# Kernel tuning notes

Measured on AMD Instinct MI355X. Metric: run time of the kernel, lower is better.

The kernel has to match this reference:

```python
import jax, jax.numpy as jnp
import numpy as np

N = 100000
E = 1600000
F_IN = 128
H1, C1 = 8, 8          # conv1: heads=8, hidden_channels=8 -> concat dim 64
H2, C2 = 1, 40         # conv2: heads=1, out=num_classes=40, concat=False
NEG_SLOPE = 0.2
EPS = 1e-16


def setup_inputs() -> dict:
    key = jax.random.key(0)
    ks = jax.random.split(key, 10)
    x = jax.random.normal(ks[0], (N, F_IN), dtype=jnp.float32)
    edge_index = jax.random.randint(ks[1], (2, E), 0, N, dtype=jnp.int32)
    s1 = 1.0 / np.sqrt(F_IN)
    s2 = 1.0 / np.sqrt(H1 * C1)
    W1 = jax.random.normal(ks[2], (F_IN, H1 * C1), dtype=jnp.float32) * s1
    att_src1 = jax.random.normal(ks[3], (H1, C1), dtype=jnp.float32) * s2
    att_dst1 = jax.random.normal(ks[4], (H1, C1), dtype=jnp.float32) * s2
    b1 = jnp.zeros((H1 * C1,), dtype=jnp.float32)
    W2 = jax.random.normal(ks[5], (H1 * C1, H2 * C2), dtype=jnp.float32) * s2
    att_src2 = jax.random.normal(ks[6], (H2, C2), dtype=jnp.float32) * (1.0 / np.sqrt(C2))
    att_dst2 = jax.random.normal(ks[7], (H2, C2), dtype=jnp.float32) * (1.0 / np.sqrt(C2))
    b2 = jnp.zeros((C2,), dtype=jnpp_zeros_dtype()) if False else jnp.zeros((C2,), dtype=jnp.float32)
    return {"x": x, "W1": W1, "att_src1": att_src1, "att_dst1": att_dst1, "b1": b1,
            "W2": W2, "att_src2": att_src2, "att_dst2": att_dst2, "b2": b2,
            "edge_index": edge_index}


def _gat_conv(x, W, att_src, att_dst, bias, src, dst, num_nodes, concat):
    """PyG GATConv (eval mode, self-loops already added to src/dst)."""
    H, C = att_src.shape
    h = (x @ W).reshape(num_nodes, H, C)                 # [N, H, C]
    a_src = jnp.sum(h * att_src[None], axis=-1)          # [N, H]
    a_dst = jnp.sum(h * att_dst[None], axis=-1)          # [N, H]
    e = a_src[src] + a_dst[dst]                          # [Etot, H]
    e = jax.nn.leaky_relu(e, NEG_SLOPE)
    # segment softmax over incoming edges of each dst node
    e_max = jax.ops.segment_max(e, dst, num_segments=num_nodes)   # [N, H]
    ex = jnp.exp(e - e_max[dst])
    denom = jax.ops.segment_sum(ex, dst, num_segments=num_nodes)  # [N, H]
    alpha = ex / (denom[dst] + EPS)                      # [Etot, H]
    msg = h[src] * alpha[..., None]                      # [Etot, H, C]
    out = jax.ops.segment_sum(msg, dst, num_segments=num_nodes)   # [N, H, C]
    if concat:
        out = out.reshape(num_nodes, H * C)
    else:
        out = out.mean(axis=1)
    return out + bias


def reference(x, W1, att_src1, att_dst1, b1, W2, att_src2, att_dst2, b2, edge_index):
    # add self-loops (PyG GATConv default add_self_loops=True)
    loops = jnp.arange(N, dtype=edge_index.dtype)
    src = jnp.concatenate([edge_index[0], loops])
    dst = jnp.concatenate([edge_index[1], loops])
    # dropout layers are identity in eval mode
    emb = jax.nn.elu(_gat_conv(x, W1, att_src1, att_dst1, b1, src, dst, N, True))
    logits = _gat_conv(emb, W2, att_src2, att_dst2, b2, src, dst, N, False)
    return jax.nn.log_softmax(logits, axis=1), emb


def jnp_zeros_dtype():
    return jnp.float32
```

## Files before the change

kernel.cpp:

```cpp
#include <hip/hip_runtime.h>
#include <hip/hip_fp16.h>
#include <math.h>

#define NN 100000
#define EE 1600000
#define ET (EE + NN)
#define FIN 128
#define D1 64
#define H1 8
#define C1 8
#define C2 40
#define NEG 0.2f
#define EPSV 1e-16f
#define LOG2E 1.4426950408889634f

#define NBKT 196
#define BCAP 10240
#define CHUNK 8192
#define NBB ((ET + CHUNK - 1) / CHUNK)

typedef _Float16 f16x8 __attribute__((ext_vector_type(8)));
typedef float f32x4 __attribute__((ext_vector_type(4)));

__device__ __forceinline__ void edge_sd(int e, const int* __restrict__ ei, int& s, int& d) {
  if (e < EE) { s = ei[e]; d = ei[EE + e]; }
  else        { s = e - EE; d = s; }
}

__global__ __launch_bounds__(256) void scatter_kernel(const int* __restrict__ ei,
                                                      int* __restrict__ gcur,
                                                      int* __restrict__ ecsr) {
  __shared__ int lh[NBKT], lres[NBKT], lcur[NBKT];
  int t = threadIdx.x;
  if (t < NBKT) { lh[t] = 0; lcur[t] = 0; }
  __syncthreads();
  int e0 = blockIdx.x * CHUNK;
  int e1 = min(e0 + CHUNK, ET);
  for (int e = e0 + t; e < e1; e += 256) {
    int d = (e < EE) ? ei[EE + e] : e - EE;
    atomicAdd(&lh[d >> 9], 1);
  }
  __syncthreads();
  if (t < NBKT && lh[t]) lres[t] = atomicAdd(&gcur[t], lh[t]);
  __syncthreads();
  for (int e = e0 + t; e < e1; e += 256) {
    int s, d; edge_sd(e, ei, s, d);
    int b = d >> 9;
    int lp = atomicAdd(&lcur[b], 1);
    ecsr[b * BCAP + lres[b] + lp] = s | ((d & 511) << 17);
  }
}

__global__ __launch_bounds__(256) void bucket2csr_kernel(const int* __restrict__ gcur,
                                                         int2* __restrict__ rowrng,
                                                         int* __restrict__ ecsr) {
  __shared__ int ebuf[BCAP];
  __shared__ int hist[512];
  __shared__ int sd[256];
  int b = blockIdx.x, t = threadIdx.x;
  int base = b * BCAP;
  int cnt = gcur[b];
  hist[t] = 0; hist[t + 256] = 0;
  __syncthreads();
  for (int i = t; i < cnt; i += 256) {
    int p = ecsr[base + i];
    ebuf[i] = p;
    atomicAdd(&hist[p >> 17], 1);
  }
  __syncthreads();
  int h0 = hist[2 * t], h1 = hist[2 * t + 1], s = h0 + h1;
  sd[t] = s;
  __syncthreads();
  for (int off = 1; off < 256; off <<= 1) {
    int x = sd[t];
    int y = (t >= off) ? sd[t - off] : 0;
    __syncthreads();
    sd[t] = x + y;
    __syncthreads();
  }
  int run = sd[t] - s;
  int g = b * 512 + 2 * t;
  if (g < NN)     rowrng[g]     = make_int2(base + run,      base + run + h0);
  if (g + 1 < NN) rowrng[g + 1] = make_int2(base + run + h0, base + run + h0 + h1);
  hist[2 * t] = run;
  hist[2 * t + 1] = run + h0;
  __syncthreads();
  for (int i = t; i < cnt; i += 256) {
    int p = ebuf[i];
    int pos = atomicAdd(&hist[p >> 17], 1);
    ecsr[base + pos] = p & 0x1FFFF;
  }
}

__global__ __launch_bounds__(256) void prep_kernel(
    const float* __restrict__ W1, const float* __restrict__ as1, const float* __restrict__ ad1,
    const float* __restrict__ W2, const float* __restrict__ as2, const float* __restrict__ ad2w,
    __half* __restrict__ Wf1, __half* __restrict__ Wf2) {
  int gid = blockIdx.x * 256 + threadIdx.x;
  int stride = gridDim.x * 256;
  for (int idx = gid; idx < 4 * 5 * 64 * 8; idx += stride) {
    int j = idx & 7, l = (idx >> 3) & 63;
    int g = idx >> 9;
    int ct = g % 5, kk = g / 5;
    int kdim = kk * 32 + (l >> 4) * 8 + j;
    int c = l & 15;
    float v;
    if (ct < 4) v = W1[kdim * 64 + ct * 16 + c];
    else {
      const float* aw = (c < 8) ? as1 : ad1;
      int hh = c & 7;
      float acc = 0.f;
      for (int q = 0; q < 8; ++q) acc += W1[kdim * 64 + hh * 8 + q] * aw[hh * 8 + q];
      v = acc * LOG2E;
    }
    Wf1[idx] = __float2half(v);
  }
  for (int idx = gid; idx < 2 * 3 * 64 * 8; idx += stride) {
    int j = idx & 7, l = (idx >> 3) & 63;
    int g = idx >> 9;
    int ct = g % 3, kk = g / 3;
    int kdim = kk * 32 + (l >> 4) * 8 + j;
    int c = ct * 16 + (l & 15);
    float v = 0.f;
    if (c < C2) v = W2[kdim * C2 + c];
    else if (c == 40 || c == 41) {
      const float* aw = (c == 40) ? as2 : ad2w;
      float acc = 0.f;
      for (int q = 0; q < C2; ++q) acc += W2[kdim * C2 + q] * aw[q];
      v = acc * LOG2E;
    }
    Wf2[idx] = __float2half(v);
  }
}

__global__ __launch_bounds__(256) void gemm1_kernel(
    const float* __restrict__ x, const __half* __restrict__ Wf1,
    __half* __restrict__ h, __half* __restrict__ as_h, float* __restrict__ ad) {
  int t = threadIdx.x;
  int w = t >> 6, lane = t & 63;
  int col = lane & 15, kg = lane >> 4;
  int node0 = blockIdx.x * 64 + w * 16;
  int nodeA = min(node0 + col, NN - 1);
  const float* xr = x + (size_t)nodeA * FIN + kg * 8;
  const f16x8* Wq = (const f16x8*)Wf1;
  f32x4 acc0 = {0.f,0.f,0.f,0.f}, acc1 = acc0, acc2 = acc0, acc3 = acc0, acc4 = acc0;
#pragma unroll
  for (int kk = 0; kk < 4; ++kk) {
    float4 xa = *(const float4*)(xr + kk * 32);
    float4 xb = *(const float4*)(xr + kk * 32 + 4);
    f16x8 a;
    a[0] = (_Float16)xa.x; a[1] = (_Float16)xa.y; a[2] = (_Float16)xa.z; a[3] = (_Float16)xa.w;
    a[4] = (_Float16)xb.x; a[5] = (_Float16)xb.y; a[6] = (_Float16)xb.z; a[7] = (_Float16)xb.w;
    acc0 = __builtin_amdgcn_mfma_f32_16x16x32_f16(a, Wq[(kk * 5 + 0) * 64 + lane], acc0, 0, 0, 0);
    acc1 = __builtin_amdgcn_mfma_f32_16x16x32_f16(a, Wq[(kk * 5 + 1) * 64 + lane], acc1, 0, 0, 0);
    acc2 = __builtin_amdgcn_mfma_f32_16x16x32_f16(a, Wq[(kk * 5 + 2) * 64 + lane], acc2, 0, 0, 0);
    acc3 = __builtin_amdgcn_mfma_f32_16x16x32_f16(a, Wq[(kk * 5 + 3) * 64 + lane], acc3, 0, 0, 0);
    acc4 = __builtin_amdgcn_mfma_f32_16x16x32_f16(a, Wq[(kk * 5 + 4) * 64 + lane], acc4, 0, 0, 0);
  }
#pragma unroll
  for (int reg = 0; reg < 4; ++reg) {
    int nr = node0 + kg * 4 + reg;
    if (nr < NN) {
      h[(size_t)nr * 64 +  0 + col] = __float2half(acc0[reg]);
      h[(size_t)nr * 64 + 16 + col] = __float2half(acc1[reg]);
      h[(size_t)nr * 64 + 32 + col] = __float2half(acc2[reg]);
      h[(size_t)nr * 64 + 48 + col] = __float2half(acc3[reg]);
      float v = acc4[reg];
      if (col < 8) as_h[nr * 8 + col] = __float2half(v);
      else         ad[nr * 8 + col - 8] = v;
    }
  }
}

#define CONS(u, avh, valid) do { \
    float xx = __half2float(avh) + adv; xx = fmaxf(xx, NEG * xx); \
    float e = (valid) ? exp2f(xx) : 0.f; den += e; \
    float2 f; \
    f = __half22float2(*(const __half2*)&(u).x); a0 = fmaf(f.x, e, a0); a1 = fmaf(f.y, e, a1); \
    f = __half22float2(*(const __half2*)&(u).y); a2 = fmaf(f.x, e, a2); a3 = fmaf(f.y, e, a3); \
    f = __half22float2(*(const __half2*)&(u).z); a4 = fmaf(f.x, e, a4); a5 = fmaf(f.y, e, a5); \
    f = __half22float2(*(const __half2*)&(u).w); a6 = fmaf(f.x, e, a6); a7 = fmaf(f.y, e, a7); \
  } while (0)

__global__ __launch_bounds__(256) void agg1_kernel(
    const int2* __restrict__ rowrng, const int* __restrict__ csr,
    const __half* __restrict__ as_h, const float* __restrict__ ad,
    const __half* __restrict__ h, const float* __restrict__ b1,
    float* __restrict__ emb) {
  int t = threadIdx.x;
  int lane = t & 63;
  int o = lane >> 3, k = lane & 7, ob = lane & 56;
  int node = blockIdx.x * 32 + (t >> 6) * 8 + o;
  int2 rr = rowrng[node];
  int beg = rr.x, deg = rr.y - rr.x, degm1 = deg - 1;
  float adv = ad[node * 8 + k];
  float den = 0.f;
  float a0=0.f,a1=0.f,a2=0.f,a3=0.f,a4=0.f,a5=0.f,a6=0.f,a7=0.f;
  uint4 uA[8]; __half vA[8]; int sjA[8];
  int sA = csr[beg + min(k, degm1)];
#pragma unroll
  for (int r = 0; r < 8; ++r) sjA[r] = __shfl(sA, ob + r, 64);
#pragma unroll
  for (int r = 0; r < 8; ++r) {
    uA[r] = *(const uint4*)(h + ((size_t)(uint)sjA[r] << 6) + (k << 3));
    vA[r] = as_h[(uint)sjA[r] * 8u + k];
  }
  for (int i = 0; i < deg; i += 16) {
    int sB = csr[beg + min(i + 8 + k, degm1)];
    int sjB[8];
#pragma unroll
    for (int r = 0; r < 8; ++r) sjB[r] = __shfl(sB, ob + r, 64);
    uint4 uB[8]; __half vB[8];
#pragma unroll
    for (int r = 0; r < 8; ++r) {
      uB[r] = *(const uint4*)(h + ((size_t)(uint)sjB[r] << 6) + (k << 3));
      vB[r] = as_h[(uint)sjB[r] * 8u + k];
    }
#pragma unroll
    for (int r = 0; r < 8; ++r) CONS(uA[r], vA[r], i + r < deg);
    int sA2 = csr[beg + min(i + 16 + k, degm1)];
#pragma unroll
    for (int r = 0; r < 8; ++r) sjA[r] = __shfl(sA2, ob + r, 64);
#pragma unroll
    for (int r = 0; r < 8; ++r) {
      uA[r] = *(const uint4*)(h + ((size_t)(uint)sjA[r] << 6) + (k << 3));
      vA[r] = as_h[(uint)sjA[r] * 8u + k];
    }
#pragma unroll
    for (int r = 0; r < 8; ++r) CONS(uB[r], vB[r], i + 8 + r < deg);
  }
  float4 bv0 = ((const float4*)b1)[2 * k];
  float4 bv1 = ((const float4*)b1)[2 * k + 1];
  float inv = 1.0f / (den + EPSV);
  float v0 = fmaf(a0, inv, bv0.x), v1 = fmaf(a1, inv, bv0.y);
  float v2 = fmaf(a2, inv, bv0.z), v3 = fmaf(a3, inv, bv0.w);
  float v4 = fmaf(a4, inv, bv1.x), v5 = fmaf(a5, inv, bv1.y);
  float v6 = fmaf(a6, inv, bv1.z), v7 = fmaf(a7, inv, bv1.w);
  v0 = v0 > 0.f ? v0 : expm1f(v0); v1 = v1 > 0.f ? v1 : expm1f(v1);
  v2 = v2 > 0.f ? v2 : expm1f(v2); v3 = v3 > 0.f ? v3 : expm1f(v3);
  v4 = v4 > 0.f ? v4 : expm1f(v4); v5 = v5 > 0.f ? v5 : expm1f(v5);
  v6 = v6 > 0.f ? v6 : expm1f(v6); v7 = v7 > 0.f ? v7 : expm1f(v7);
  float4 s0; s0.x = v0; s0.y = v1; s0.z = v2; s0.w = v3;
  float4 s1; s1.x = v4; s1.y = v5; s1.z = v6; s1.w = v7;
  float* ep = emb + (size_t)node * D1 + (k << 3);
  ((float4*)ep)[0] = s0; ((float4*)ep)[1] = s1;
}

__global__ __launch_bounds__(256) void gemm2_kernel(
    const float* __restrict__ emb, const __half* __restrict__ Wf2,
    __half* __restrict__ h2, float* __restrict__ ad2) {
  int t = threadIdx.x;
  int w = t >> 6, lane = t & 63;
  int col = lane & 15, kg = lane >> 4;
  int node0 = blockIdx.x * 64 + w * 16;
  int nodeA = min(node0 + col, NN - 1);
  const float* er = emb + (size_t)nodeA * D1 + kg * 8;
  const f16x8* Wq = (const f16x8*)Wf2;
  f32x4 acc0 = {0.f,0.f,0.f,0.f}, acc1 = acc0, acc2 = acc0;
#pragma unroll
  for (int kk = 0; kk < 2; ++kk) {
    float4 xa = *(const float4*)(er + kk * 32);
    float4 xb = *(const float4*)(er + kk * 32 + 4);
    f16x8 a;
    a[0] = (_Float16)xa.x; a[1] = (_Float16)xa.y; a[2] = (_Float16)xa.z; a[3] = (_Float16)xa.w;
    a[4] = (_Float16)xb.x; a[5] = (_Float16)xb.y; a[6] = (_Float16)xb.z; a[7] = (_Float16)xb.w;
    acc0 = __builtin_amdgcn_mfma_f32_16x16x32_f16(a, Wq[(kk * 3 + 0) * 64 + lane], acc0, 0, 0, 0);
    acc1 = __builtin_amdgcn_mfma_f32_16x16x32_f16(a, Wq[(kk * 3 + 1) * 64 + lane], acc1, 0, 0, 0);
    acc2 = __builtin_amdgcn_mfma_f32_16x16x32_f16(a, Wq[(kk * 3 + 2) * 64 + lane], acc2, 0, 0, 0);
  }
#pragma unroll
  for (int reg = 0; reg < 4; ++reg) {
    int nr = node0 + kg * 4 + reg;
    if (nr < NN) {
      h2[(size_t)nr * 64 +  0 + col] = __float2half(acc0[reg]);
      h2[(size_t)nr * 64 + 16 + col] = __float2half(acc1[reg]);
      float v = acc2[reg];
      if (col < 8)       h2[(size_t)nr * 64 + 32 + col] = __float2half(v);
      else if (col == 8) h2[(size_t)nr * 64 + 40] = __float2half(v);
      else if (col == 9) ad2[nr] = v;
    }
  }
}

__global__ __launch_bounds__(256) void agg2_kernel(
    const int2* __restrict__ rowrng, const int* __restrict__ csr,
    const float* __restrict__ ad, const __half* __restrict__ h2,
    const float* __restrict__ b2, float* __restrict__ out) {
  int t = threadIdx.x;
  int lane = t & 63;
  int o = lane >> 3, k = lane & 7, ob = lane & 56;
  int kc = min(k, 4);
  int node = blockIdx.x * 32 + (t >> 6) * 8 + o;
  int2 rr = rowrng[node];
  int beg = rr.x, deg = rr.y - rr.x, degm1 = deg - 1;
  float adv = ad[node];
  float den = 0.f;
  float a0=0.f,a1=0.f,a2=0.f,a3=0.f,a4=0.f,a5=0.f,a6=0.f,a7=0.f;
  uint4 uA[8]; __half vA[8]; int sjA[8];
  int sA = csr[beg + min(k, degm1)];
#pragma unroll
  for (int r = 0; r < 8; ++r) sjA[r] = __shfl(sA, ob + r, 64);
#pragma unroll
  for (int r = 0; r < 8; ++r) {
    const __half* rp = h2 + ((size_t)(uint)sjA[r] << 6);
    uA[r] = *(const uint4*)(rp + (kc << 3));
    vA[r] = rp[40];
  }
  for (int i = 0; i < deg; i += 16) {
    int sB = csr[beg + min(i + 8 + k, degm1)];
    int sjB[8];
#pragma unroll
    for (int r = 0; r < 8; ++r) sjB[r] = __shfl(sB, ob + r, 64);
    uint4 uB[8]; __half vB[8];
#pragma unroll
    for (int r = 0; r < 8; ++r) {
      const __half* rp = h2 + ((size_t)(uint)sjB[r] << 6);
      uB[r] = *(const uint4*)(rp + (kc << 3));
      vB[r] = rp[40];
    }
#pragma unroll
    for (int r = 0; r < 8; ++r) CONS(uA[r], vA[r], i + r < deg);
    int sA2 = csr[beg + min(i + 16 + k, degm1)];
#pragma unroll
    for (int r = 0; r < 8; ++r) sjA[r] = __shfl(sA2, ob + r, 64);
#pragma unroll
    for (int r = 0; r < 8; ++r) {
      const __half* rp = h2 + ((size_t)(uint)sjA[r] << 6);
      uA[r] = *(const uint4*)(rp + (kc << 3));
      vA[r] = rp[40];
    }
#pragma unroll
    for (int r = 0; r < 8; ++r) CONS(uB[r], vB[r], i + 8 + r < deg);
  }
  float4 bv0 = ((const float4*)b2)[2 * kc];
  float4 bv1 = ((const float4*)b2)[2 * kc + 1];
  float inv = 1.0f / (den + EPSV);
  float v0 = fmaf(a0, inv, bv0.x), v1 = fmaf(a1, inv, bv0.y);
  float v2 = fmaf(a2, inv, bv0.z), v3 = fmaf(a3, inv, bv0.w);
  float v4 = fmaf(a4, inv, bv1.x), v5 = fmaf(a5, inv, bv1.y);
  float v6 = fmaf(a6, inv, bv1.z), v7 = fmaf(a7, inv, bv1.w);
  bool act = (k < 5);
  float m = act ? fmaxf(fmaxf(fmaxf(v0, v1), fmaxf(v2, v3)),
                        fmaxf(fmaxf(v4, v5), fmaxf(v6, v7))) : -INFINITY;
#pragma unroll
  for (int off = 1; off < 8; off <<= 1) m = fmaxf(m, __shfl_xor(m, off, 64));
  float ex = act ? (__expf(v0 - m) + __expf(v1 - m) + __expf(v2 - m) + __expf(v3 - m) +
                    __expf(v4 - m) + __expf(v5 - m) + __expf(v6 - m) + __expf(v7 - m)) : 0.f;
#pragma unroll
  for (int off = 1; off < 8; off <<= 1) ex += __shfl_xor(ex, off, 64);
  if (act) {
    float lls = m + logf(ex);
    float4 s0; s0.x = v0 - lls; s0.y = v1 - lls; s0.z = v2 - lls; s0.w = v3 - lls;
    float4 s1; s1.x = v4 - lls; s1.y = v5 - lls; s1.z = v6 - lls; s1.w = v7 - lls;
    float* op = out + (size_t)node * C2 + (k << 3);
    ((float4*)op)[0] = s0; ((float4*)op)[1] = s1;
  }
}

extern "C" void kernel_launch(void* const* d_in, const int* in_sizes, int n_in,
                              void* d_out, int out_size, void* d_ws, size_t ws_size,
                              hipStream_t stream) {
  const float* x    = (const float*)d_in[0];
  const float* W1   = (const float*)d_in[1];
  const float* as1w = (const float*)d_in[2];
  const float* ad1w = (const float*)d_in[3];
  const float* b1   = (const float*)d_in[4];
  const float* W2   = (const float*)d_in[5];
  const float* as2w = (const float*)d_in[6];
  const float* ad2w = (const float*)d_in[7];
  const float* b2   = (const float*)d_in[8];
  const int*   ei   = (const int*)d_in[9];

  float* out   = (float*)d_out;
  float* outls = out;
  float* emb   = out + (long)NN * C2;

  char* wsb = (char*)d_ws;
  __half* h1   = (__half*)wsb; wsb += sizeof(__half) * (size_t)NN * D1;
  __half* h2   = (__half*)wsb; wsb += sizeof(__half) * ((size_t)NN * 64 + 64);
  __half* ash1 = (__half*)wsb; wsb += sizeof(__half) * (size_t)NN * H1;
  float* adst1 = (float*)wsb; wsb += sizeof(float) * (size_t)NN * H1;
  float* adst2 = (float*)wsb; wsb += sizeof(float) * (size_t)NN;
  int2* rowrng = (int2*)wsb;  wsb += sizeof(int2) * (size_t)NN;
  int* gcur    = (int*)wsb;   wsb += sizeof(int) * (NBKT + 4);
  __half* Wf1  = (__half*)wsb; wsb += sizeof(__half) * 4 * 5 * 64 * 8;
  __half* Wf2  = (__half*)wsb; wsb += sizeof(__half) * 2 * 3 * 64 * 8;
  int* ecsr    = (int*)wsb;   wsb += sizeof(int) * (size_t)NBKT * BCAP;

  prep_kernel<<<16, 256, 0, stream>>>(W1, as1w, ad1w, W2, as2w, ad2w, Wf1, Wf2);
  hipMemsetAsync(gcur, 0, sizeof(int) * (NBKT + 4), stream);
  scatter_kernel<<<NBB, 256, 0, stream>>>(ei, gcur, ecsr);
  bucket2csr_kernel<<<NBKT, 256, 0, stream>>>(gcur, rowrng, ecsr);

  gemm1_kernel<<<(NN + 63) / 64, 256, 0, stream>>>(x, Wf1, h1, ash1, adst1);
  agg1_kernel<<<NN / 32, 256, 0, stream>>>(rowrng, ecsr, ash1, adst1, h1, b1, emb);

  gemm2_kernel<<<(NN + 63) / 64, 256, 0, stream>>>(emb, Wf2, h2, adst2);
  agg2_kernel<<<NN / 32, 256, 0, stream>>>(rowrng, ecsr, adst2, h2, b2, outls);
}
```

Measured before the change: 264.7 us.

## Merge preprocessing launches into two heterogeneous kernels and shrink CSR buckets

```diff
diff --git a/kernel.cpp b/kernel.cpp
--- a/kernel.cpp
+++ b/kernel.cpp
@@ -14,10 +14,12 @@
 #define EPSV 1e-16f
 #define LOG2E 1.4426950408889634f
 
-#define NBKT 196
-#define BCAP 10240
-#define CHUNK 8192
+#define NBKT 391
+#define BCAP 5120
+#define CHUNK 2048
 #define NBB ((ET + CHUNK - 1) / CHUNK)
+#define G1B ((NN + 63) / 64)
+#define PREPB 16
 
 typedef _Float16 f16x8 __attribute__((ext_vector_type(8)));
 typedef float f32x4 __attribute__((ext_vector_type(4)));
@@ -27,147 +29,145 @@
   else        { s = e - EE; d = s; }
 }
 
-__global__ __launch_bounds__(256) void scatter_kernel(const int* __restrict__ ei,
-                                                      int* __restrict__ gcur,
-                                                      int* __restrict__ ecsr) {
-  __shared__ int lh[NBKT], lres[NBKT], lcur[NBKT];
-  int t = threadIdx.x;
-  if (t < NBKT) { lh[t] = 0; lcur[t] = 0; }
-  __syncthreads();
-  int e0 = blockIdx.x * CHUNK;
-  int e1 = min(e0 + CHUNK, ET);
-  for (int e = e0 + t; e < e1; e += 256) {
-    int d = (e < EE) ? ei[EE + e] : e - EE;
-    atomicAdd(&lh[d >> 9], 1);
-  }
-  __syncthreads();
-  if (t < NBKT && lh[t]) lres[t] = atomicAdd(&gcur[t], lh[t]);
-  __syncthreads();
-  for (int e = e0 + t; e < e1; e += 256) {
-    int s, d; edge_sd(e, ei, s, d);
-    int b = d >> 9;
-    int lp = atomicAdd(&lcur[b], 1);
-    ecsr[b * BCAP + lres[b] + lp] = s | ((d & 511) << 17);
-  }
-}
-
-__global__ __launch_bounds__(256) void bucket2csr_kernel(const int* __restrict__ gcur,
-                                                         int2* __restrict__ rowrng,
-                                                         int* __restrict__ ecsr) {
-  __shared__ int ebuf[BCAP];
-  __shared__ int hist[512];
-  __shared__ int sd[256];
-  int b = blockIdx.x, t = threadIdx.x;
-  int base = b * BCAP;
-  int cnt = gcur[b];
-  hist[t] = 0; hist[t + 256] = 0;
-  __syncthreads();
-  for (int i = t; i < cnt; i += 256) {
-    int p = ecsr[base + i];
-    ebuf[i] = p;
-    atomicAdd(&hist[p >> 17], 1);
-  }
-  __syncthreads();
-  int h0 = hist[2 * t], h1 = hist[2 * t + 1], s = h0 + h1;
-  sd[t] = s;
-  __syncthreads();
-  for (int off = 1; off < 256; off <<= 1) {
-    int x = sd[t];
-    int y = (t >= off) ? sd[t - off] : 0;
-    __syncthreads();
-    sd[t] = x + y;
-    __syncthreads();
-  }
-  int run = sd[t] - s;
-  int g = b * 512 + 2 * t;
-  if (g < NN)     rowrng[g]     = make_int2(base + run,      base + run + h0);
-  if (g + 1 < NN) rowrng[g + 1] = make_int2(base + run + h0, base + run + h0 + h1);
-  hist[2 * t] = run;
-  hist[2 * t + 1] = run + h0;
-  __syncthreads();
-  for (int i = t; i < cnt; i += 256) {
-    int p = ebuf[i];
-    int pos = atomicAdd(&hist[p >> 17], 1);
-    ecsr[base + pos] = p & 0x1FFFF;
-  }
-}
-
-__global__ __launch_bounds__(256) void prep_kernel(
+__global__ __launch_bounds__(256) void k1_kernel(
+    const int* __restrict__ ei, int* __restrict__ gcur, int* __restrict__ ecsr,
     const float* __restrict__ W1, const float* __restrict__ as1, const float* __restrict__ ad1,
     const float* __restrict__ W2, const float* __restrict__ as2, const float* __restrict__ ad2w,
     __half* __restrict__ Wf1, __half* __restrict__ Wf2) {
-  int gid = blockIdx.x * 256 + threadIdx.x;
-  int stride = gridDim.x * 256;
-  for (int idx = gid; idx < 4 * 5 * 64 * 8; idx += stride) {
-    int j = idx & 7, l = (idx >> 3) & 63;
-    int g = idx >> 9;
-    int ct = g % 5, kk = g / 5;
-    int kdim = kk * 32 + (l >> 4) * 8 + j;
-    int c = l & 15;
-    float v;
-    if (ct < 4) v = W1[kdim * 64 + ct * 16 + c];
-    else {
-      const float* aw = (c < 8) ? as1 : ad1;
-      int hh = c & 7;
-      float acc = 0.f;
-      for (int q = 0; q < 8; ++q) acc += W1[kdim * 64 + hh * 8 + q] * aw[hh * 8 + q];
-      v = acc * LOG2E;
-    }
-    Wf1[idx] = __float2half(v);
-  }
-  for (int idx = gid; idx < 2 * 3 * 64 * 8; idx += stride) {
-    int j = idx & 7, l = (idx >> 3) & 63;
-    int g = idx >> 9;
-    int ct = g % 3, kk = g / 3;
-    int kdim = kk * 32 + (l >> 4) * 8 + j;
-    int c = ct * 16 + (l & 15);
-    float v = 0.f;
-    if (c < C2) v = W2[kdim * C2 + c];
-    else if (c == 40 || c == 41) {
-      const float* aw = (c == 40) ? as2 : ad2w;
-      float acc = 0.f;
-      for (int q = 0; q < C2; ++q) acc += W2[kdim * C2 + q] * aw[q];
-      v = acc * LOG2E;
-    }
-    Wf2[idx] = __float2half(v);
-  }
-}
-
-__global__ __launch_bounds__(256) void gemm1_kernel(
+  __shared__ int lh[NBKT], lres[NBKT], lcur[NBKT];
+  int t = threadIdx.x;
+  if (blockIdx.x < NBB) {
+    for (int i = t; i < NBKT; i += 256) { lh[i] = 0; lcur[i] = 0; }
+    __syncthreads();
+    int e0 = blockIdx.x * CHUNK;
+    int e1 = min(e0 + CHUNK, ET);
+    for (int e = e0 + t; e < e1; e += 256) {
+      int d = (e < EE) ? ei[EE + e] : e - EE;
+      atomicAdd(&lh[d >> 8], 1);
+    }
+    __syncthreads();
+    for (int i = t; i < NBKT; i += 256)
+      if (lh[i]) lres[i] = atomicAdd(&gcur[i], lh[i]);
+    __syncthreads();
+    for (int e = e0 + t; e < e1; e += 256) {
+      int s, d; edge_sd(e, ei, s, d);
+      int b = d >> 8;
+      int lp = atomicAdd(&lcur[b], 1);
+      ecsr[b * BCAP + lres[b] + lp] = s | ((d & 255) << 17);
+    }
+  } else {
+    int gid = (blockIdx.x - NBB) * 256 + t;
+    int stride = PREPB * 256;
+    for (int idx = gid; idx < 4 * 5 * 64 * 8; idx += stride) {
+      int j = idx & 7, l = (idx >> 3) & 63;
+      int g = idx >> 9;
+      int ct = g % 5, kk = g / 5;
+      int kdim = kk * 32 + (l >> 4) * 8 + j;
+      int c = l & 15;
+      float v;
+      if (ct < 4) v = W1[kdim * 64 + ct * 16 + c];
+      else {
+        const float* aw = (c < 8) ? as1 : ad1;
+        int hh = c & 7;
+        float acc = 0.f;
+        for (int q = 0; q < 8; ++q) acc += W1[kdim * 64 + hh * 8 + q] * aw[hh * 8 + q];
+        v = acc * LOG2E;
+      }
+      Wf1[idx] = __float2half(v);
+    }
+    for (int idx = gid; idx < 2 * 3 * 64 * 8; idx += stride) {
+      int j = idx & 7, l = (idx >> 3) & 63;
+      int g = idx >> 9;
+      int ct = g % 3, kk = g / 3;
+      int kdim = kk * 32 + (l >> 4) * 8 + j;
+      int c = ct * 16 + (l & 15);
+      float v = 0.f;
+      if (c < C2) v = W2[kdim * C2 + c];
+      else if (c == 40 || c == 41) {
+        const float* aw = (c == 40) ? as2 : ad2w;
+        float acc = 0.f;
+        for (int q = 0; q < C2; ++q) acc += W2[kdim * C2 + q] * aw[q];
+        v = acc * LOG2E;
+      }
+      Wf2[idx] = __float2half(v);
+    }
+  }
+}
+
+__global__ __launch_bounds__(256) void k2_kernel(
+    const int* __restrict__ gcur, int2* __restrict__ rowrng, int* __restrict__ ecsr,
     const float* __restrict__ x, const __half* __restrict__ Wf1,
     __half* __restrict__ h, __half* __restrict__ as_h, float* __restrict__ ad) {
+  __shared__ int ebuf[BCAP];
+  __shared__ int hist[256];
+  __shared__ int sd[256];
   int t = threadIdx.x;
-  int w = t >> 6, lane = t & 63;
-  int col = lane & 15, kg = lane >> 4;
-  int node0 = blockIdx.x * 64 + w * 16;
-  int nodeA = min(node0 + col, NN - 1);
-  const float* xr = x + (size_t)nodeA * FIN + kg * 8;
-  const f16x8* Wq = (const f16x8*)Wf1;
-  f32x4 acc0 = {0.f,0.f,0.f,0.f}, acc1 = acc0, acc2 = acc0, acc3 = acc0, acc4 = acc0;
-#pragma unroll
-  for (int kk = 0; kk < 4; ++kk) {
-    float4 xa = *(const float4*)(xr + kk * 32);
-    float4 xb = *(const float4*)(xr + kk * 32 + 4);
-    f16x8 a;
-    a[0] = (_Float16)xa.x; a[1] = (_Float16)xa.y; a[2] = (_Float16)xa.z; a[3] = (_Float16)xa.w;
-    a[4] = (_Float16)xb.x; a[5] = (_Float16)xb.y; a[6] = (_Float16)xb.z; a[7] = (_Float16)xb.w;
-    acc0 = __builtin_amdgcn_mfma_f32_16x16x32_f16(a, Wq[(kk * 5 + 0) * 64 + lane], acc0, 0, 0, 0);
-    acc1 = __builtin_amdgcn_mfma_f32_16x16x32_f16(a, Wq[(kk * 5 + 1) * 64 + lane], acc1, 0, 0, 0);
-    acc2 = __builtin_amdgcn_mfma_f32_16x16x32_f16(a, Wq[(kk * 5 + 2) * 64 + lane], acc2, 0, 0, 0);
-    acc3 = __builtin_amdgcn_mfma_f32_16x16x32_f16(a, Wq[(kk * 5 + 3) * 64 + lane], acc3, 0, 0, 0);
-    acc4 = __builtin_amdgcn_mfma_f32_16x16x32_f16(a, Wq[(kk * 5 + 4) * 64 + lane], acc4, 0, 0, 0);
-  }
-#pragma unroll
-  for (int reg = 0; reg < 4; ++reg) {
-    int nr = node0 + kg * 4 + reg;
-    if (nr < NN) {
-      h[(size_t)nr * 64 +  0 + col] = __float2half(acc0[reg]);
-      h[(size_t)nr * 64 + 16 + col] = __float2half(acc1[reg]);
-      h[(size_t)nr * 64 + 32 + col] = __float2half(acc2[reg]);
-      h[(size_t)nr * 64 + 48 + col] = __float2half(acc3[reg]);
-      float v = acc4[reg];
-      if (col < 8) as_h[nr * 8 + col] = __float2half(v);
-      else         ad[nr * 8 + col - 8] = v;
+  if (blockIdx.x < NBKT) {
+    int b = blockIdx.x;
+    int base = b * BCAP;
+    int cnt = gcur[b];
+    hist[t] = 0;
+    __syncthreads();
+    for (int i = t; i < cnt; i += 256) {
+      int p = ecsr[base + i];
+      ebuf[i] = p;
+      atomicAdd(&hist[p >> 17], 1);
+    }
+    __syncthreads();
+    int h0 = hist[t];
+    sd[t] = h0;
+    __syncthreads();
+    for (int off = 1; off < 256; off <<= 1) {
+      int xv = sd[t];
+      int yv = (t >= off) ? sd[t - off] : 0;
+      __syncthreads();
+      sd[t] = xv + yv;
+      __syncthreads();
+    }
+    int run = sd[t] - h0;
+    int g = b * 256 + t;
+    if (g < NN) rowrng[g] = make_int2(base + run, base + run + h0);
+    hist[t] = run;
+    __syncthreads();
+    for (int i = t; i < cnt; i += 256) {
+      int p = ebuf[i];
+      int pos = atomicAdd(&hist[p >> 17], 1);
+      ecsr[base + pos] = p & 0x1FFFF;
+    }
+  } else {
+    int blk = blockIdx.x - NBKT;
+    int w = t >> 6, lane = t & 63;
+    int col = lane & 15, kg = lane >> 4;
+    int node0 = blk * 64 + w * 16;
+    int nodeA = min(node0 + col, NN - 1);
+    const float* xr = x + (size_t)nodeA * FIN + kg * 8;
+    const f16x8* Wq = (const f16x8*)Wf1;
+    f32x4 acc0 = {0.f,0.f,0.f,0.f}, acc1 = acc0, acc2 = acc0, acc3 = acc0, acc4 = acc0;
+#pragma unroll
+    for (int kk = 0; kk < 4; ++kk) {
+      float4 xa = *(const float4*)(xr + kk * 32);
+      float4 xb = *(const float4*)(xr + kk * 32 + 4);
+      f16x8 a;
+      a[0] = (_Float16)xa.x; a[1] = (_Float16)xa.y; a[2] = (_Float16)xa.z; a[3] = (_Float16)xa.w;
+      a[4] = (_Float16)xb.x; a[5] = (_Float16)xb.y; a[6] = (_Float16)xb.z; a[7] = (_Float16)xb.w;
+      acc0 = __builtin_amdgcn_mfma_f32_16x16x32_f16(a, Wq[(kk * 5 + 0) * 64 + lane], acc0, 0, 0, 0);
+      acc1 = __builtin_amdgcn_mfma_f32_16x16x32_f16(a, Wq[(kk * 5 + 1) * 64 + lane], acc1, 0, 0, 0);
+      acc2 = __builtin_amdgcn_mfma_f32_16x16x32_f16(a, Wq[(kk * 5 + 2) * 64 + lane], acc2, 0, 0, 0);
+      acc3 = __builtin_amdgcn_mfma_f32_16x16x32_f16(a, Wq[(kk * 5 + 3) * 64 + lane], acc3, 0, 0, 0);
+      acc4 = __builtin_amdgcn_mfma_f32_16x16x32_f16(a, Wq[(kk * 5 + 4) * 64 + lane], acc4, 0, 0, 0);
+    }
+#pragma unroll
+    for (int reg = 0; reg < 4; ++reg) {
+      int nr = node0 + kg * 4 + reg;
+      if (nr < NN) {
+        h[(size_t)nr * 64 +  0 + col] = __float2half(acc0[reg]);
+        h[(size_t)nr * 64 + 16 + col] = __float2half(acc1[reg]);
+        h[(size_t)nr * 64 + 32 + col] = __float2half(acc2[reg]);
+        h[(size_t)nr * 64 + 48 + col] = __float2half(acc3[reg]);
+        float v = acc4[reg];
+        if (col < 8) as_h[nr * 8 + col] = __float2half(v);
+        else         ad[nr * 8 + col - 8] = v;
+      }
     }
   }
 }
@@ -196,38 +196,43 @@
   float adv = ad[node * 8 + k];
   float den = 0.f;
   float a0=0.f,a1=0.f,a2=0.f,a3=0.f,a4=0.f,a5=0.f,a6=0.f,a7=0.f;
-  uint4 uA[8]; __half vA[8]; int sjA[8];
-  int sA = csr[beg + min(k, degm1)];
-#pragma unroll
-  for (int r = 0; r < 8; ++r) sjA[r] = __shfl(sA, ob + r, 64);
-#pragma unroll
-  for (int r = 0; r < 8; ++r) {
-    uA[r] = *(const uint4*)(h + ((size_t)(uint)sjA[r] << 6) + (k << 3));
-    vA[r] = as_h[(uint)sjA[r] * 8u + k];
+  uint4 uA[8]; __half vA[8];
+  {
+    int sA = csr[beg + min(k, degm1)];
+#pragma unroll
+    for (int r = 0; r < 8; ++r) {
+      int sj = __shfl(sA, ob + r, 64);
+      uA[r] = *(const uint4*)(h + ((size_t)(uint)sj << 6) + (k << 3));
+      vA[r] = as_h[(uint)sj * 8u + k];
+    }
   }
   for (int i = 0; i < deg; i += 16) {
-    int sB = csr[beg + min(i + 8 + k, degm1)];
-    int sjB[8];
-#pragma unroll
-    for (int r = 0; r < 8; ++r) sjB[r] = __shfl(sB, ob + r, 64);
     uint4 uB[8]; __half vB[8];
-#pragma unroll
-    for (int r = 0; r < 8; ++r) {
-      uB[r] = *(const uint4*)(h + ((size_t)(uint)sjB[r] << 6) + (k << 3));
-      vB[r] = as_h[(uint)sjB[r] * 8u + k];
+    bool haveB = (i + 8 < deg);
+    if (haveB) {
+      int sB = csr[beg + min(i + 8 + k, degm1)];
+#pragma unroll
+      for (int r = 0; r < 8; ++r) {
+        int sj = __shfl(sB, ob + r, 64);
+        uB[r] = *(const uint4*)(h + ((size_t)(uint)sj << 6) + (k << 3));
+        vB[r] = as_h[(uint)sj * 8u + k];
+      }
     }
 #pragma unroll
     for (int r = 0; r < 8; ++r) CONS(uA[r], vA[r], i + r < deg);
-    int sA2 = csr[beg + min(i + 16 + k, degm1)];
-#pragma unroll
-    for (int r = 0; r < 8; ++r) sjA[r] = __shfl(sA2, ob + r, 64);
-#pragma unroll
-    for (int r = 0; r < 8; ++r) {
-      uA[r] = *(const uint4*)(h + ((size_t)(uint)sjA[r] << 6) + (k << 3));
-      vA[r] = as_h[(uint)sjA[r] * 8u + k];
-    }
-#pragma unroll
-    for (int r = 0; r < 8; ++r) CONS(uB[r], vB[r], i + 8 + r < deg);
+    if (i + 16 < deg) {
+      int sA2 = csr[beg + min(i + 16 + k, degm1)];
+#pragma unroll
+      for (int r = 0; r < 8; ++r) {
+        int sj = __shfl(sA2, ob + r, 64);
+        uA[r] = *(const uint4*)(h + ((size_t)(uint)sj << 6) + (k << 3));
+        vA[r] = as_h[(uint)sj * 8u + k];
+      }
+    }
+    if (haveB) {
+#pragma unroll
+      for (int r = 0; r < 8; ++r) CONS(uB[r], vB[r], i + 8 + r < deg);
+    }
   }
   float4 bv0 = ((const float4*)b1)[2 * k];
   float4 bv1 = ((const float4*)b1)[2 * k + 1];
@@ -296,41 +301,46 @@
   float adv = ad[node];
   float den = 0.f;
   float a0=0.f,a1=0.f,a2=0.f,a3=0.f,a4=0.f,a5=0.f,a6=0.f,a7=0.f;
-  uint4 uA[8]; __half vA[8]; int sjA[8];
-  int sA = csr[beg + min(k, degm1)];
-#pragma unroll
-  for (int r = 0; r < 8; ++r) sjA[r] = __shfl(sA, ob + r, 64);
-#pragma unroll
-  for (int r = 0; r < 8; ++r) {
-    const __half* rp = h2 + ((size_t)(uint)sjA[r] << 6);
-    uA[r] = *(const uint4*)(rp + (kc << 3));
-    vA[r] = rp[40];
-  }
-  for (int i = 0; i < deg; i += 16) {
-    int sB = csr[beg + min(i + 8 + k, degm1)];
-    int sjB[8];
-#pragma unroll
-    for (int r = 0; r < 8; ++r) sjB[r] = __shfl(sB, ob + r, 64);
-    uint4 uB[8]; __half vB[8];
+  uint4 uA[8]; __half vA[8];
+  {
+    int sA = csr[beg + min(k, degm1)];
 #pragma unroll
     for (int r = 0; r < 8; ++r) {
-      const __half* rp = h2 + ((size_t)(uint)sjB[r] << 6);
-      uB[r] = *(const uint4*)(rp + (kc << 3));
-      vB[r] = rp[40];
-    }
-#pragma unroll
-    for (int r = 0; r < 8; ++r) CONS(uA[r], vA[r], i + r < deg);
-    int sA2 = csr[beg + min(i + 16 + k, degm1)];
-#pragma unroll
-    for (int r = 0; r < 8; ++r) sjA[r] = __shfl(sA2, ob + r, 64);
-#pragma unroll
-    for (int r = 0; r < 8; ++r) {
-      const __half* rp = h2 + ((size_t)(uint)sjA[r] << 6);
+      int sj = __shfl(sA, ob + r, 64);
+      const __half* rp = h2 + ((size_t)(uint)sj << 6);
       uA[r] = *(const uint4*)(rp + (kc << 3));
       vA[r] = rp[40];
     }
-#pragma unroll
-    for (int r = 0; r < 8; ++r) CONS(uB[r], vB[r], i + 8 + r < deg);
+  }
+  for (int i = 0; i < deg; i += 16) {
+    uint4 uB[8]; __half vB[8];
+    bool haveB = (i + 8 < deg);
+    if (haveB) {
+      int sB = csr[beg + min(i + 8 + k, degm1)];
+#pragma unroll
+      for (int r = 0; r < 8; ++r) {
+        int sj = __shfl(sB, ob + r, 64);
+        const __half* rp = h2 + ((size_t)(uint)sj << 6);
+        uB[r] = *(const uint4*)(rp + (kc << 3));
+        vB[r] = rp[40];
+      }
+    }
+#pragma unroll
+    for (int r = 0; r < 8; ++r) CONS(uA[r], vA[r], i + r < deg);
+    if (i + 16 < deg) {
+      int sA2 = csr[beg + min(i + 16 + k, degm1)];
+#pragma unroll
+      for (int r = 0; r < 8; ++r) {
+        int sj = __shfl(sA2, ob + r, 64);
+        const __half* rp = h2 + ((size_t)(uint)sj << 6);
+        uA[r] = *(const uint4*)(rp + (kc << 3));
+        vA[r] = rp[40];
+      }
+    }
+    if (haveB) {
+#pragma unroll
+      for (int r = 0; r < 8; ++r) CONS(uB[r], vB[r], i + 8 + r < deg);
+    }
   }
   float4 bv0 = ((const float4*)b2)[2 * kc];
   float4 bv1 = ((const float4*)b2)[2 * kc + 1];
@@ -387,14 +397,11 @@
   __half* Wf2  = (__half*)wsb; wsb += sizeof(__half) * 2 * 3 * 64 * 8;
   int* ecsr    = (int*)wsb;   wsb += sizeof(int) * (size_t)NBKT * BCAP;
 
-  prep_kernel<<<16, 256, 0, stream>>>(W1, as1w, ad1w, W2, as2w, ad2w, Wf1, Wf2);
   hipMemsetAsync(gcur, 0, sizeof(int) * (NBKT + 4), stream);
-  scatter_kernel<<<NBB, 256, 0, stream>>>(ei, gcur, ecsr);
-  bucket2csr_kernel<<<NBKT, 256, 0, stream>>>(gcur, rowrng, ecsr);
-
-  gemm1_kernel<<<(NN + 63) / 64, 256, 0, stream>>>(x, Wf1, h1, ash1, adst1);
+  k1_kernel<<<NBB + PREPB, 256, 0, stream>>>(ei, gcur, ecsr,
+                                             W1, as1w, ad1w, W2, as2w, ad2w, Wf1, Wf2);
+  k2_kernel<<<NBKT + G1B, 256, 0, stream>>>(gcur, rowrng, ecsr, x, Wf1, h1, ash1, adst1);
   agg1_kernel<<<NN / 32, 256, 0, stream>>>(rowrng, ecsr, ash1, adst1, h1, b1, emb);
-
   gemm2_kernel<<<(NN + 63) / 64, 256, 0, stream>>>(emb, Wf2, h2, adst2);
   agg2_kernel<<<NN / 32, 256, 0, stream>>>(rowrng, ecsr, adst2, h2, b2, outls);
 }
```

After: 257.5 us. -2.7%, faster.
